# Optimization experiments

Measured on AMD Instinct MI355X. Metric: run time of the kernel, lower is better.

Reference implementation:

```python
import jax, jax.numpy as jnp
import numpy as np
import itertools

N_PTS = 256
NUM_HEADS = 8
DIMENSION = 32
LEVELS = DIMENSION // 2          # feature_dim=2 per level
FEAT = 2
TABLE = 4096                     # hashtable_size = 2**12
N_MIN, N_MAX = 1.0, 20.0         # int(1/0.05) = 20
N_ENC = 3 * NUM_HEADS

_b = (N_MAX / N_MIN) ** (1.0 / (LEVELS - 1))
RES = np.floor(N_MIN * _b ** np.arange(LEVELS)).astype(np.float32)  # per-level grid resolution
PRIMES = jnp.array([1, 2654435761, 805459861], dtype=jnp.uint32)    # instant-NGP spatial hash primes


def _hash(c):
    # c: uint32 [..., 3] integer grid coords (negatives wrap harmlessly in uint32)
    h = (c[..., 0] * PRIMES[0]) ^ (c[..., 1] * PRIMES[1]) ^ (c[..., 2] * PRIMES[2])
    return (h % TABLE).astype(jnp.int32)


def _encode_all(tables, pts):
    # tables: [E, L, T, F]; pts: [P, 3] -> [E, P, L*F]
    res = jnp.asarray(RES)
    scaled = pts[None, :, :] * res[:, None, None]      # [L, P, 3]
    base = jnp.floor(scaled)
    w = scaled - base                                  # trilinear fractions [L, P, 3]
    c0 = base.astype(jnp.int32)
    L, P = scaled.shape[0], scaled.shape[1]
    larange = jnp.arange(L)[:, None]
    acc = jnp.zeros((tables.shape[0], L, P, FEAT), tables.dtype)
    for off in itertools.product((0, 1), repeat=3):    # 8 cube corners (fixed small loop)
        offa = jnp.array(off, jnp.int32)
        idx = _hash((c0 + offa).astype(jnp.uint32))    # [L, P]
        weight = jnp.prod(jnp.where(offa.astype(bool), w, 1.0 - w), axis=-1)  # [L, P]
        feats = tables[:, larange, idx, :]             # gather -> [E, L, P, F]
        acc = acc + weight[None, :, :, None] * feats
    # concat level features: [E, P, L*F]
    return acc.transpose(0, 2, 1, 3).reshape(tables.shape[0], P, L * FEAT)


def setup_inputs() -> dict:
    key = jax.random.key(0)
    k1, k2 = jax.random.split(key)
    xyz = jax.random.uniform(k1, (N_PTS, 3), dtype=jnp.float32)
    # learned hashtables for all 3*num_heads encoders, NGP-style small uniform init
    tables = (jax.random.uniform(k2, (N_ENC, LEVELS, TABLE, FEAT), dtype=jnp.float32) * 2.0 - 1.0) * 1e-4
    return {"xyz": xyz, "tables": tables}


def reference(xyz, tables):
    n = xyz.shape[0]
    rel = (xyz[:, None, :] - xyz[None, :, :]).reshape(-1, 3)   # [N*N, 3]
    enc = _encode_all(tables, rel)                             # [3*H, N*N, D]
    out = enc.reshape(3, NUM_HEADS, n, n, LEVELS * FEAT)       # encoder e = i*H + h
    return (out[0], out[1], out[2])
```

## Files before the change

### kernel.cpp

```cpp
#include <hip/hip_runtime.h>
#include <hip/hip_fp16.h>

#define NPTS 256
#define TABLE 4096
#define N_ENC 24
#define P_TOTAL (NPTS * NPTS)
#define PRIME1 2654435761u
#define PRIME2 805459861u
#define ENTRY_H2 32
#define N_CENT 28211

typedef float f32x4 __attribute__((ext_vector_type(4)));


__global__ __launch_bounds__(256) void k_build(const float2* __restrict__ src,
                                               __half2* __restrict__ T2) {
    const int tid = blockIdx.x * 256 + threadIdx.x;
    if (tid >= N_CENT * N_ENC) return;
    const int t = tid % N_ENC;
    const int e = tid / N_ENC;
    constexpr int B[17] = {0,27,54,81,108,233,358,701,1430,2159,4356,
                           7731,11827,15923,20019,24115,28211};
    constexpr int Rv[16] = {1,1,1,1,2,2,3,4,4,6,7,8,10,13,16,19};
#pragma unroll
    for (int l = 0; l < 16; ++l) {
        if (e >= B[l] && e < B[l + 1]) {
            const int local = e - B[l];
            int hash;
            if (l <= 10) {
                const int R = Rv[l], D = 2 * R + 1;
                const int x = local / (D * D), rem = local - x * (D * D);
                const int y = rem / D, z = rem - y * D;
                hash = (int)((((unsigned)(x - R))
                            ^ ((unsigned)(y - R)) * PRIME1
                            ^ ((unsigned)(z - R)) * PRIME2) & (TABLE - 1u));
            } else {
                hash = local;
            }
            const float2 f = src[((t * 16 + l) * TABLE) + hash];
            T2[(size_t)e * ENTRY_H2 + t] =
                __halves2half2(__float2half_rn(f.x), __float2half_rn(f.y));
        }
    }
}

__global__ __launch_bounds__(256) void k_main(const float* __restrict__ xyz,
                                              const char* __restrict__ Tb,
                                              float* __restrict__ out) {
    const int lane = threadIdx.x & 63;
    const int p = blockIdx.x * 4 + (threadIdx.x >> 6);
    const int i = p >> 8, j = p & 255;
    const int l8 = lane >> 3;
    const int q  = lane & 7;

    const float rx = xyz[i * 3 + 0] - xyz[j * 3 + 0];
    const float ry = xyz[i * 3 + 1] - xyz[j * 3 + 1];
    const float rz = xyz[i * 3 + 2] - xyz[j * 3 + 2];

    const unsigned long long RESLO = 0x0403020201010101ull;
    const unsigned long long RESHI = 0x13100D0A08070604ull;
    const unsigned long long DLO   = 0x0907050503030303ull;
    const unsigned long long DHI   = 0x00000000000F0D09ull;
    const unsigned long long C0    = 0x00510036001B0000ull;
    const unsigned long long C1    = 0x02BD016600E9006Cull;
    const unsigned long long C2    = 0x1E331104086F0596ull;
    const unsigned long long C3    = 0x5E334E333E332E33ull;

    __half2 pwh[2][4], zuh[2], zwh[2];
    unsigned offs[16];
#pragma unroll
    for (int h = 0; h < 2; ++h) {
        const int level = 2 * l8 + h;
        const unsigned shift8 = (level & 7) * 8;
        const float res = (float)((((l8 < 4) ? RESLO : RESHI) >> shift8) & 0xFF);
        const int   R   = (int)res;
        const int   D   = (int)((((l8 < 4) ? DLO : DHI) >> shift8) & 0xFF);
        const unsigned long long Bw = (l8 < 2) ? C0 : (l8 < 4) ? C1
                                    : (l8 < 6) ? C2 : C3;
        const unsigned base = (unsigned)((Bw >> ((level & 3) * 16)) & 0xFFFF);
        const bool latt = (l8 <= 5 - h);

        const float sx = rx * res, sy = ry * res, sz = rz * res;
        const float bx = floorf(sx), by = floorf(sy), bz = floorf(sz);
        const float wxx = sx - bx, wyy = sy - by, wzz = sz - bz;
        const float uxx = 1.0f - wxx, uyy = 1.0f - wyy, uzz = 1.0f - wzz;
        pwh[h][0] = __float2half2_rn(uxx * uyy);
        pwh[h][1] = __float2half2_rn(wxx * uyy);
        pwh[h][2] = __float2half2_rn(uxx * wyy);
        pwh[h][3] = __float2half2_rn(wxx * wyy);
        zuh[h] = __float2half2_rn(uzz);
        zwh[h] = __float2half2_rn(wzz);

        const int bxi = (int)bx, byi = (int)by, bzi = (int)bz;
        const unsigned hx0 = (unsigned)bxi,          hx1 = hx0 + 1u;
        const unsigned hy0 = (unsigned)byi * PRIME1, hy1 = hy0 + PRIME1;
        const unsigned hz0 = (unsigned)bzi * PRIME2, hz1 = hz0 + PRIME2;
        const unsigned hbase = (base << 7) + ((unsigned)q << 4);
        const int iA = ((bxi + R) * D + (byi + R)) * D + (bzi + R);
        const unsigned addrC = ((base + (unsigned)iA) << 7) + ((unsigned)q << 4);
        const unsigned DDs = (unsigned)(D * D) << 7;
        const unsigned Dbs = (unsigned)D << 7;

#pragma unroll
        for (int c = 0; c < 8; ++c) {
            unsigned offC = addrC;
            if (c & 1) offC += DDs;
            if (c & 2) offC += Dbs;
            if (c & 4) offC += 128u;
            const unsigned hsh = ((c & 1) ? hx1 : hx0)
                               ^ ((c & 2) ? hy1 : hy0)
                               ^ ((c & 4) ? hz1 : hz0);
            const unsigned offH = hbase + ((hsh & (TABLE - 1u)) << 7);
            offs[c * 2 + h] = latt ? offC : offH;
        }
    }

    int4 raw[16];
#pragma unroll
    for (int k = 0; k < 8; ++k)
        raw[k] = *(const int4*)(Tb + offs[k]);

    __half2 accA[4] = {}, accB[4] = {};
#pragma unroll
    for (int k = 0; k < 16; ++k) {
        if (k < 8)
            raw[k + 8] = *(const int4*)(Tb + offs[k + 8]);
        const int c = k >> 1, h = k & 1;
        const __half2 wh = __hmul2(pwh[h][c & 3], (c & 4) ? zwh[h] : zuh[h]);
        __half2* acc = h ? accB : accA;
        const int* cb = &raw[k].x;
#pragma unroll
        for (int r = 0; r < 4; ++r) {
            __half2 hv;
            __builtin_memcpy(&hv, &cb[r], 4);
            acc[r] = __hfma2(hv, wh, acc[r]);
        }
    }

    if (q < 6) {
#pragma unroll
        for (int r = 0; r < 4; ++r) {
            const int t = 4 * q + r;
            const float2 a = __half22float2(accA[r]);
            const float2 b = __half22float2(accB[r]);
            f32x4 v;
            v.x = a.x; v.y = a.y; v.z = b.x; v.w = b.y;
            float* dst = out + (size_t)t * ((size_t)P_TOTAL * 32)
                             + (size_t)p * 32 + 4 * l8;
            __builtin_nontemporal_store(v, (f32x4*)dst);
        }
    }
}

extern "C" void kernel_launch(void* const* d_in, const int* in_sizes, int n_in,
                              void* d_out, int out_size, void* d_ws, size_t ws_size,
                              hipStream_t stream) {
    const float* xyz    = (const float*)d_in[0];
    const float* tables = (const float*)d_in[1];
    float* out = (float*)d_out;

    const int nb = (N_CENT * N_ENC + 255) / 256;
    k_build<<<nb, 256, 0, stream>>>((const float2*)tables, (__half2*)d_ws);
    k_main<<<P_TOTAL / 4, 256, 0, stream>>>(xyz, (const char*)d_ws, out);
}
```

Before: 72.99 us.

## Stage coarse-level tables in LDS and process multiple points per block

Each block now copies the first ~45KB of the packed half table (the coarse levels used by lanes with l8<3) into shared memory and reads those corners from LDS instead of global memory. Blocks process 64 points in a loop instead of 4, so the copy cost is spread over more work and the xi coordinates are loaded once. The price is a per-block copy plus a barrier, high LDS use that limits how many blocks fit per CU, and far fewer blocks in the grid.

New measurement: 141.8 us. +94.2%, slower.

```diff
diff --git a/kernel.cpp b/kernel.cpp
--- a/kernel.cpp
+++ b/kernel.cpp
@@ -9,7 +9,10 @@
 #define PRIME2 805459861u
 #define ENTRY_H2 32
 #define N_CENT 28211
+#define S_BYTES 45824
+#define PTS_PER_BLK 64
 
+typedef int   i32x4 __attribute__((ext_vector_type(4)));
 typedef float f32x4 __attribute__((ext_vector_type(4)));
 
 
@@ -47,15 +50,19 @@
 __global__ __launch_bounds__(256) void k_main(const float* __restrict__ xyz,
                                               const char* __restrict__ Tb,
                                               float* __restrict__ out) {
+    __shared__ __align__(16) char s_tab[S_BYTES];
+    for (int n = threadIdx.x; n < S_BYTES / 16; n += 256)
+        ((i32x4*)s_tab)[n] = ((const i32x4*)Tb)[n];
+    __syncthreads();
+
     const int lane = threadIdx.x & 63;
-    const int p = blockIdx.x * 4 + (threadIdx.x >> 6);
-    const int i = p >> 8, j = p & 255;
+    const int w    = threadIdx.x >> 6;
     const int l8 = lane >> 3;
     const int q  = lane & 7;
 
-    const float rx = xyz[i * 3 + 0] - xyz[j * 3 + 0];
-    const float ry = xyz[i * 3 + 1] - xyz[j * 3 + 1];
-    const float rz = xyz[i * 3 + 2] - xyz[j * 3 + 2];
+    const int pbase = blockIdx.x * PTS_PER_BLK;
+    const int i = pbase >> 8;
+    const float xi = xyz[3 * i], yi = xyz[3 * i + 1], zi = xyz[3 * i + 2];
 
     const unsigned long long RESLO = 0x0403020201010101ull;
     const unsigned long long RESHI = 0x13100D0A08070604ull;
@@ -66,88 +73,100 @@
     const unsigned long long C2    = 0x1E331104086F0596ull;
     const unsigned long long C3    = 0x5E334E333E332E33ull;
 
-    __half2 pwh[2][4], zuh[2], zwh[2];
-    unsigned offs[16];
+#pragma unroll 1
+    for (int it = 0; it < PTS_PER_BLK / 4; ++it) {
+        const int p = pbase + w * (PTS_PER_BLK / 4) + it;
+        const int j = p & 255;
+        const float rx = xi - xyz[3 * j + 0];
+        const float ry = yi - xyz[3 * j + 1];
+        const float rz = zi - xyz[3 * j + 2];
+
+        __half2 pwh[2][4], zuh[2], zwh[2];
+        unsigned offs[16];
 #pragma unroll
-    for (int h = 0; h < 2; ++h) {
-        const int level = 2 * l8 + h;
-        const unsigned shift8 = (level & 7) * 8;
-        const float res = (float)((((l8 < 4) ? RESLO : RESHI) >> shift8) & 0xFF);
-        const int   R   = (int)res;
-        const int   D   = (int)((((l8 < 4) ? DLO : DHI) >> shift8) & 0xFF);
-        const unsigned long long Bw = (l8 < 2) ? C0 : (l8 < 4) ? C1
-                                    : (l8 < 6) ? C2 : C3;
-        const unsigned base = (unsigned)((Bw >> ((level & 3) * 16)) & 0xFFFF);
-        const bool latt = (l8 <= 5 - h);
+        for (int h = 0; h < 2; ++h) {
+            const int level = 2 * l8 + h;
+            const unsigned shift8 = (level & 7) * 8;
+            const float res = (float)((((l8 < 4) ? RESLO : RESHI) >> shift8) & 0xFF);
+            const int   R   = (int)res;
+            const int   D   = (int)((((l8 < 4) ? DLO : DHI) >> shift8) & 0xFF);
+            const unsigned long long Bw = (l8 < 2) ? C0 : (l8 < 4) ? C1
+                                        : (l8 < 6) ? C2 : C3;
+            const unsigned base = (unsigned)((Bw >> ((level & 3) * 16)) & 0xFFFF);
+            const bool latt = (l8 <= 5 - h);
 
-        const float sx = rx * res, sy = ry * res, sz = rz * res;
-        const float bx = floorf(sx), by = floorf(sy), bz = floorf(sz);
-        const float wxx = sx - bx, wyy = sy - by, wzz = sz - bz;
-        const float uxx = 1.0f - wxx, uyy = 1.0f - wyy, uzz = 1.0f - wzz;
-        pwh[h][0] = __float2half2_rn(uxx * uyy);
-        pwh[h][1] = __float2half2_rn(wxx * uyy);
-        pwh[h][2] = __float2half2_rn(uxx * wyy);
-        pwh[h][3] = __float2half2_rn(wxx * wyy);
-        zuh[h] = __float2half2_rn(uzz);
-        zwh[h] = __float2half2_rn(wzz);
+            const float sx = rx * res, sy = ry * res, sz = rz * res;
+            const float bx = floorf(sx), by = floorf(sy), bz = floorf(sz);
+            const float wxx = sx - bx, wyy = sy - by, wzz = sz - bz;
+            const float uxx = 1.0f - wxx, uyy = 1.0f - wyy, uzz = 1.0f - wzz;
+            pwh[h][0] = __float2half2_rn(uxx * uyy);
+            pwh[h][1] = __float2half2_rn(wxx * uyy);
+            pwh[h][2] = __float2half2_rn(uxx * wyy);
+            pwh[h][3] = __float2half2_rn(wxx * wyy);
+            zuh[h] = __float2half2_rn(uzz);
+            zwh[h] = __float2half2_rn(wzz);
 
-        const int bxi = (int)bx, byi = (int)by, bzi = (int)bz;
-        const unsigned hx0 = (unsigned)bxi,          hx1 = hx0 + 1u;
-        const unsigned hy0 = (unsigned)byi * PRIME1, hy1 = hy0 + PRIME1;
-        const unsigned hz0 = (unsigned)bzi * PRIME2, hz1 = hz0 + PRIME2;
-        const unsigned hbase = (base << 7) + ((unsigned)q << 4);
-        const int iA = ((bxi + R) * D + (byi + R)) * D + (bzi + R);
-        const unsigned addrC = ((base + (unsigned)iA) << 7) + ((unsigned)q << 4);
-        const unsigned DDs = (unsigned)(D * D) << 7;
-        const unsigned Dbs = (unsigned)D << 7;
+            const int bxi = (int)bx, byi = (int)by, bzi = (int)bz;
+            const unsigned hx0 = (unsigned)bxi,          hx1 = hx0 + 1u;
+            const unsigned hy0 = (unsigned)byi * PRIME1, hy1 = hy0 + PRIME1;
+            const unsigned hz0 = (unsigned)bzi * PRIME2, hz1 = hz0 + PRIME2;
+            const unsigned hbase = (base << 7) + ((unsigned)q << 4);
+            const int iA = ((bxi + R) * D + (byi + R)) * D + (bzi + R);
+            const unsigned addrC = ((base + (unsigned)iA) << 7) + ((unsigned)q << 4);
+            const unsigned DDs = (unsigned)(D * D) << 7;
+            const unsigned Dbs = (unsigned)D << 7;
 
 #pragma unroll
-        for (int c = 0; c < 8; ++c) {
-            unsigned offC = addrC;
-            if (c & 1) offC += DDs;
-            if (c & 2) offC += Dbs;
-            if (c & 4) offC += 128u;
-            const unsigned hsh = ((c & 1) ? hx1 : hx0)
-                               ^ ((c & 2) ? hy1 : hy0)
-                               ^ ((c & 4) ? hz1 : hz0);
-            const unsigned offH = hbase + ((hsh & (TABLE - 1u)) << 7);
-            offs[c * 2 + h] = latt ? offC : offH;
+            for (int c = 0; c < 8; ++c) {
+                unsigned offC = addrC;
+                if (c & 1) offC += DDs;
+                if (c & 2) offC += Dbs;
+                if (c & 4) offC += 128u;
+                const unsigned hsh = ((c & 1) ? hx1 : hx0)
+                                   ^ ((c & 2) ? hy1 : hy0)
+                                   ^ ((c & 4) ? hz1 : hz0);
+                const unsigned offH = hbase + ((hsh & (TABLE - 1u)) << 7);
+                offs[c * 2 + h] = latt ? offC : offH;
+            }
         }
-    }
 
-    int4 raw[16];
+        i32x4 raw[16];
 #pragma unroll
-    for (int k = 0; k < 8; ++k)
-        raw[k] = *(const int4*)(Tb + offs[k]);
+        for (int k = 0; k < 8; ++k) {
+            if (l8 < 3) raw[k] = *(const i32x4*)(s_tab + offs[k]);
+            else        raw[k] = *(const i32x4*)(Tb + offs[k]);
+        }
 
-    __half2 accA[4] = {}, accB[4] = {};
+        __half2 accA[4] = {}, accB[4] = {};
 #pragma unroll
-    for (int k = 0; k < 16; ++k) {
-        if (k < 8)
-            raw[k + 8] = *(const int4*)(Tb + offs[k + 8]);
-        const int c = k >> 1, h = k & 1;
-        const __half2 wh = __hmul2(pwh[h][c & 3], (c & 4) ? zwh[h] : zuh[h]);
-        __half2* acc = h ? accB : accA;
-        const int* cb = &raw[k].x;
+        for (int k = 0; k < 16; ++k) {
+            if (k < 8) {
+                if (l8 < 3) raw[k + 8] = *(const i32x4*)(s_tab + offs[k + 8]);
+                else        raw[k + 8] = *(const i32x4*)(Tb + offs[k + 8]);
+            }
+            const int c = k >> 1, h = k & 1;
+            const __half2 wh = __hmul2(pwh[h][c & 3], (c & 4) ? zwh[h] : zuh[h]);
+            __half2* acc = h ? accB : accA;
 #pragma unroll
-        for (int r = 0; r < 4; ++r) {
-            __half2 hv;
-            __builtin_memcpy(&hv, &cb[r], 4);
-            acc[r] = __hfma2(hv, wh, acc[r]);
+            for (int r = 0; r < 4; ++r) {
+                __half2 hv;
+                __builtin_memcpy(&hv, (const char*)&raw[k] + 4 * r, 4);
+                acc[r] = __hfma2(hv, wh, acc[r]);
+            }
         }
-    }
 
-    if (q < 6) {
+        if (q < 6) {
 #pragma unroll
-        for (int r = 0; r < 4; ++r) {
-            const int t = 4 * q + r;
-            const float2 a = __half22float2(accA[r]);
-            const float2 b = __half22float2(accB[r]);
-            f32x4 v;
-            v.x = a.x; v.y = a.y; v.z = b.x; v.w = b.y;
-            float* dst = out + (size_t)t * ((size_t)P_TOTAL * 32)
-                             + (size_t)p * 32 + 4 * l8;
-            __builtin_nontemporal_store(v, (f32x4*)dst);
+            for (int r = 0; r < 4; ++r) {
+                const int t = 4 * q + r;
+                const float2 a = __half22float2(accA[r]);
+                const float2 b = __half22float2(accB[r]);
+                f32x4 v;
+                v.x = a.x; v.y = a.y; v.z = b.x; v.w = b.y;
+                float* dst = out + (size_t)t * ((size_t)P_TOTAL * 32)
+                                 + (size_t)p * 32 + 4 * l8;
+                __builtin_nontemporal_store(v, (f32x4*)dst);
+            }
         }
     }
 }
@@ -161,5 +180,5 @@
 
     const int nb = (N_CENT * N_ENC + 255) / 256;
     k_build<<<nb, 256, 0, stream>>>((const float2*)tables, (__half2*)d_ws);
-    k_main<<<P_TOTAL / 4, 256, 0, stream>>>(xyz, (const char*)d_ws, out);
+    k_main<<<P_TOTAL / PTS_PER_BLK, 256, 0, stream>>>(xyz, (const char*)d_ws, out);
 }
```
